# Optimization experiments

Hardware: AMD Instinct MI355X
Metric: run time of the kernel (lower is better)

Reference implementation:

```python
import jax, jax.numpy as jnp
import numpy as np

T, H, I, E, K = 4096, 1024, 768, 8, 2

def setup_inputs() -> dict:
    key = jax.random.key(0)
    k1, k2, k3, k4 = jax.random.split(key, 4)
    s_h = 1.0 / np.sqrt(H)
    s_i = 1.0 / np.sqrt(I)
    return {
        "hidden_states": jax.random.normal(k1, (T, H), dtype=jnp.float32),
        "gate_w": jax.random.normal(k2, (E, H), dtype=jnp.float32) * s_h,   # router, fp32
        "w13": jax.random.normal(k3, (E, 2 * I, H), dtype=jnp.float32) * s_h,  # fused gate+up
        "w2": jax.random.normal(k4, (E, H, I), dtype=jnp.float32) * s_i,
        "num_global_tokens": T,
        "max_num_tokens_per_gpu": T,
    }

def reference(hidden_states, gate_w, w13, w2, num_global_tokens, max_num_tokens_per_gpu):
    x = hidden_states  # [T, H]
    orig_dtype = x.dtype
    # router runs in fp32 (router_dtype == 'float32')
    router_logits = jnp.einsum('th,eh->te', x.astype(jnp.float32), gate_w)
    router_logits = router_logits.astype(orig_dtype)
    # FusedMoE top-k: softmax in fp32 over all experts, then top-k; renormalize=False
    probs = jax.nn.softmax(router_logits.astype(jnp.float32), axis=-1)  # [T, E]
    topk_w, topk_ids = jax.lax.top_k(probs, K)  # [T, K]
    # dense combine weights [T, E] (scatter of top-k weights)
    combine = jnp.sum(jax.nn.one_hot(topk_ids, E, dtype=topk_w.dtype) * topk_w[..., None], axis=1)
    combine = combine.astype(orig_dtype)
    # dense per-expert SwiGLU MLP, masked-combined (grouped GEMM reference)
    h = jnp.einsum('th,ejh->tej', x, w13)  # [T, E, 2I]
    g, u = h[..., :I], h[..., I:]
    a = jax.nn.silu(g) * u                 # [T, E, I]
    o = jnp.einsum('tei,ehi->teh', a, w2)  # [T, E, H]
    out = jnp.einsum('teh,te->th', o, combine)  # routed_scaling_factor = 1.0
    return out.reshape(x.shape)
```

## Files before the change

### kernel.cpp

```cpp
#include <hip/hip_runtime.h>
#include <hip/hip_bf16.h>

#define TT 4096
#define HH 1024
#define II 768
#define EE 8
#define TWOI 1536

typedef __attribute__((ext_vector_type(8))) short bf16x8;
typedef __attribute__((ext_vector_type(8))) unsigned short u16x8;
typedef __attribute__((ext_vector_type(4))) float f32x4;

__device__ unsigned short g_x_bf[TT * HH];
__device__ unsigned short g_w13_bf[EE * TWOI * HH];
__device__ unsigned short g_w2_bf[EE * HH * II];
__device__ unsigned short g_a[EE * TT * II];
__device__ unsigned short g_opart[2 * TT * HH];
__device__ int g_perm_tok[EE * TT];
__device__ float g_perm_w[EE * TT];
__device__ int g_perm_slot[EE * TT];
__device__ int g_cnt[EE];
__device__ int g_e1[TT];
__device__ int g_e2[TT];
__device__ float g_w1f[TT];
__device__ float g_w2f[TT];

__device__ __forceinline__ unsigned short f2bf(float f) {
  union { float f; unsigned u; } v; v.f = f;
  unsigned r = v.u + 0x7fff + ((v.u >> 16) & 1);
  return (unsigned short)(r >> 16);
}

__device__ __forceinline__ float bf2f(unsigned short u) {
  union { unsigned v; float f; } c; c.v = (unsigned)u << 16; return c.f;
}

__device__ __forceinline__ void gload16(const void* g, void* l) {
  __builtin_amdgcn_global_load_lds(
      (const __attribute__((address_space(1))) void*)g,
      (__attribute__((address_space(3))) void*)l, 16, 0, 0);
}

__device__ __forceinline__ void cvt_sub(const float* __restrict__ inb,
                                        unsigned short* __restrict__ dstb,
                                        long rowbase, int nrowf,
                                        long chunkbase, char* lds) {
  const int tid = threadIdx.x;
  const int wv = tid >> 6;
  const int lane = tid & 63;
#pragma unroll
  for (int i = 0; i < 4; ++i) {
    int r = i * 4 + wv;
    const float* src = inb + (rowbase + r) * (size_t)nrowf + lane * 4;
    gload16(src, lds + r * 1040);
  }
  asm volatile("s_waitcnt vmcnt(0)" ::: "memory");
  __syncthreads();
#pragma unroll
  for (int it = 0; it < 2; ++it) {
    int kb = it * 4 + wv;
    int g = lane;
    int r = g & 15, c8 = g >> 4;
    const float* lf = (const float*)(lds + r * 1040) + kb * 32 + c8 * 8;
    float4 a = ((const float4*)lf)[0];
    float4 c = ((const float4*)lf)[1];
    u16x8 o;
    o[0] = f2bf(a.x); o[1] = f2bf(a.y); o[2] = f2bf(a.z); o[3] = f2bf(a.w);
    o[4] = f2bf(c.x); o[5] = f2bf(c.y); o[6] = f2bf(c.z); o[7] = f2bf(c.w);
    *(u16x8*)(dstb + (chunkbase + kb) * 512 + (size_t)g * 8) = o;
  }
}

__global__ __launch_bounds__(256) void k_prep(const float* __restrict__ x,
                                              const float* __restrict__ gw,
                                              const float* __restrict__ w13,
                                              const float* __restrict__ w2) {
  __shared__ char lds[16640];
  const int b = blockIdx.x;
  const int wv = threadIdx.x >> 6;
  const int lane = threadIdx.x & 63;
  if (b >= 1024) {
    if (b < 4096) {
      int s = b - 1024;
      int grp = s >> 2, sub = s & 3;
      cvt_sub(w13 + sub * 256, g_w13_bf, (long)grp * 16, HH,
              (long)grp * 32 + sub * 8, lds);
    } else {
      int s = b - 4096;
      int grp = s / 3, sub = s - grp * 3;
      cvt_sub(w2 + sub * 256, g_w2_bf, (long)grp * 16, II,
              (long)grp * 24 + sub * 8, lds);
    }
    return;
  }
  const int t = b * 4 + wv;

  const float* xr = x + (size_t)t * HH + lane * 16;
  float4 xv0 = *(const float4*)(xr + 0);
  float4 xv1 = *(const float4*)(xr + 4);
  float4 xv2 = *(const float4*)(xr + 8);
  float4 xv3 = *(const float4*)(xr + 12);

  unsigned short* xd = g_x_bf + (size_t)t * HH + lane * 16;
  ushort4 o0, o1, o2, o3;
  o0.x = f2bf(xv0.x); o0.y = f2bf(xv0.y); o0.z = f2bf(xv0.z); o0.w = f2bf(xv0.w);
  o1.x = f2bf(xv1.x); o1.y = f2bf(xv1.y); o1.z = f2bf(xv1.z); o1.w = f2bf(xv1.w);
  o2.x = f2bf(xv2.x); o2.y = f2bf(xv2.y); o2.z = f2bf(xv2.z); o2.w = f2bf(xv2.w);
  o3.x = f2bf(xv3.x); o3.y = f2bf(xv3.y); o3.z = f2bf(xv3.z); o3.w = f2bf(xv3.w);
  *(ushort4*)(xd + 0) = o0;
  *(ushort4*)(xd + 4) = o1;
  *(ushort4*)(xd + 8) = o2;
  *(ushort4*)(xd + 12) = o3;

  float lg[EE];
#pragma unroll
  for (int ei = 0; ei < EE; ++ei) {
    const float* gr = gw + ei * HH + lane * 16;
    float4 g0 = *(const float4*)(gr + 0);
    float4 g1 = *(const float4*)(gr + 4);
    float4 g2 = *(const float4*)(gr + 8);
    float4 g3 = *(const float4*)(gr + 12);
    float a = xv0.x * g0.x + xv0.y * g0.y + xv0.z * g0.z + xv0.w * g0.w
            + xv1.x * g1.x + xv1.y * g1.y + xv1.z * g1.z + xv1.w * g1.w
            + xv2.x * g2.x + xv2.y * g2.y + xv2.z * g2.z + xv2.w * g2.w
            + xv3.x * g3.x + xv3.y * g3.y + xv3.z * g3.z + xv3.w * g3.w;
#pragma unroll
    for (int s = 32; s > 0; s >>= 1) a += __shfl_xor(a, s);
    lg[ei] = a;
  }

  if (lane == 0) {
    float mx = lg[0];
#pragma unroll
    for (int ei = 1; ei < EE; ++ei) mx = fmaxf(mx, lg[ei]);
    float p[EE]; float s = 0.f;
#pragma unroll
    for (int ei = 0; ei < EE; ++ei) { p[ei] = expf(lg[ei] - mx); s += p[ei]; }
    float inv = 1.f / s;
    int e1 = 0; float b1 = lg[0];
#pragma unroll
    for (int ei = 1; ei < EE; ++ei) if (lg[ei] > b1) { b1 = lg[ei]; e1 = ei; }
    int e2 = -1; float b2 = -3.0e38f;
#pragma unroll
    for (int ei = 0; ei < EE; ++ei)
      if (ei != e1 && lg[ei] > b2) { b2 = lg[ei]; e2 = ei; }

    g_e1[t] = e1;
    g_e2[t] = e2;
    g_w1f[t] = p[e1] * inv;
    g_w2f[t] = p[e2] * inv;
  }
}

__global__ __launch_bounds__(256) void k_compact() {
  const int e = blockIdx.x;
  const int tid = threadIdx.x;
  __shared__ int pre[256];

  const int t0 = tid * (TT / 256);
  int c = 0;
#pragma unroll
  for (int j = 0; j < TT / 256; ++j) {
    int t = t0 + j;
    if (g_e1[t] == e) ++c;
    if (g_e2[t] == e) ++c;
  }
  pre[tid] = c;
  __syncthreads();
  for (int off = 1; off < 256; off <<= 1) {
    int v = (tid >= off) ? pre[tid - off] : 0;
    __syncthreads();
    pre[tid] += v;
    __syncthreads();
  }
  int pos = pre[tid] - c;
#pragma unroll
  for (int j = 0; j < TT / 256; ++j) {
    int t = t0 + j;
    if (g_e1[t] == e) {
      g_perm_tok[e * TT + pos] = t;
      g_perm_w[e * TT + pos] = g_w1f[t];
      g_perm_slot[e * TT + pos] = 0;
      ++pos;
    }
    if (g_e2[t] == e) {
      g_perm_tok[e * TT + pos] = t;
      g_perm_w[e * TT + pos] = g_w2f[t];
      g_perm_slot[e * TT + pos] = 1;
      ++pos;
    }
  }
  if (tid == 255) g_cnt[e] = pre[255];
}

__global__ __launch_bounds__(512) void k_gemm1() {
  const int bid = blockIdx.x;
  const int e = bid & 7;
  const int k = bid >> 3;
  const int cb = k % 6;
  const int rowbase = (k / 6) * 128;
  const int cnt = g_cnt[e];
  if (rowbase >= cnt) return;
  const int tid = threadIdx.x;
  const int lane = tid & 63;
  const int wid = tid >> 6;
  const int wm = wid >> 1;
  const int wc = wid & 1;

  __shared__ uint4 sA[3][512];
  __shared__ uint4 sBg[3][512];
  __shared__ uint4 sBu[3][512];

  const int r16 = lane & 15;
  const int c8 = lane >> 4;
  const int arow = rowbase + wid * 16 + r16;
  const int tok = (arow < cnt) ? g_perm_tok[e * TT + arow] : 0;
  const unsigned short* aptr = g_x_bf + (size_t)tok * HH + c8 * 8;
  const unsigned short* bgp =
      g_w13_bf + ((size_t)(e * 96 + cb * 8 + wid) * 32) * 512 + lane * 8;
  const unsigned short* bup = bgp + (size_t)48 * 32 * 512;

  const int soff = __builtin_amdgcn_readfirstlane(wid * 1024);

#define STG1(buf, kk) do { \
    gload16(aptr + (kk) * 32, (char*)sA + (buf) * 8192 + soff); \
    gload16(bgp + (size_t)(kk) * 512, (char*)sBg + (buf) * 8192 + soff); \
    gload16(bup + (size_t)(kk) * 512, (char*)sBu + (buf) * 8192 + soff); \
  } while (0)

  f32x4 accg[2][4], accu[2][4];
#pragma unroll
  for (int m = 0; m < 2; ++m)
#pragma unroll
    for (int n = 0; n < 4; ++n) {
      accg[m][n] = (f32x4){0.f, 0.f, 0.f, 0.f};
      accu[m][n] = (f32x4){0.f, 0.f, 0.f, 0.f};
    }

  STG1(0, 0);
  STG1(1, 1);
  for (int ks = 0; ks < 32; ++ks) {
    const int cur = ks % 3;
    if (ks < 30) {
      const int stg = (ks + 2) % 3;
      STG1(stg, ks + 2);
      asm volatile("s_waitcnt vmcnt(6)" ::: "memory");
    } else if (ks == 30) {
      asm volatile("s_waitcnt vmcnt(3)" ::: "memory");
    } else {
      asm volatile("s_waitcnt vmcnt(0)" ::: "memory");
    }
    __builtin_amdgcn_s_barrier();
    __builtin_amdgcn_sched_barrier(0);
    bf16x8 af[2], bgf[4], buf_[4];
#pragma unroll
    for (int m = 0; m < 2; ++m)
      af[m] = *(const bf16x8*)((const char*)sA + cur * 8192 + (wm * 2 + m) * 1024 + lane * 16);
#pragma unroll
    for (int n = 0; n < 4; ++n) {
      int jb = wc * 4 + n;
      bgf[n] = *(const bf16x8*)((const char*)sBg + cur * 8192 + jb * 1024 + lane * 16);
      buf_[n] = *(const bf16x8*)((const char*)sBu + cur * 8192 + jb * 1024 + lane * 16);
    }
#pragma unroll
    for (int m = 0; m < 2; ++m)
#pragma unroll
      for (int n = 0; n < 4; ++n) {
        accg[m][n] = __builtin_amdgcn_mfma_f32_16x16x32_bf16(af[m], bgf[n], accg[m][n], 0, 0, 0);
        accu[m][n] = __builtin_amdgcn_mfma_f32_16x16x32_bf16(af[m], buf_[n], accu[m][n], 0, 0, 0);
      }
    __builtin_amdgcn_sched_barrier(0);
    __builtin_amdgcn_s_barrier();
  }
#undef STG1

  const int rhi = lane >> 4, clo = lane & 15;
  unsigned short* abase = g_a + ((size_t)(e * 256 + (rowbase >> 4)) * 24) * 512;
#pragma unroll
  for (int m = 0; m < 2; ++m) {
#pragma unroll
    for (int jj = 0; jj < 4; ++jj) {
      int rbl = wm * 2 + m;
      int rr = rhi * 4 + jj;
      int row = rowbase + rbl * 16 + rr;
      if (row < cnt) {
#pragma unroll
        for (int n = 0; n < 4; ++n) {
          int kb = cb * 4 + wc * 2 + (n >> 1);
          int sub = (2 * n + (clo >> 3)) & 3;
          float gv = accg[m][n][jj];
          float uv = accu[m][n][jj];
          float av = gv / (1.f + __expf(-gv)) * uv;
          abase[((size_t)rbl * 24 + kb) * 512 + sub * 128 + rr * 8 + (clo & 7)] = f2bf(av);
        }
      }
    }
  }
}

__global__ __launch_bounds__(512) void k_gemm2() {
  const int bid = blockIdx.x;
  const int e = bid & 7;
  const int k = bid >> 3;
  const int cb = k % 8;
  const int rowbase = (k / 8) * 128;
  const int cnt = g_cnt[e];
  if (rowbase >= cnt) return;
  const int tid = threadIdx.x;
  const int lane = tid & 63;
  const int wid = tid >> 6;
  const int wm = wid >> 1;
  const int wc = wid & 1;

  __shared__ uint4 sA[3][512];
  __shared__ uint4 sB[3][512];
  __shared__ int s_tok[128];
  __shared__ float s_w[128];
  __shared__ int s_slot[128];

  if (tid < 128) {
    int row = rowbase + tid;
    bool v = row < cnt;
    s_tok[tid] = v ? g_perm_tok[e * TT + row] : 0;
    s_w[tid] = v ? g_perm_w[e * TT + row] : 0.f;
    s_slot[tid] = v ? g_perm_slot[e * TT + row] : 0;
  }

  const unsigned short* aptr =
      g_a + ((size_t)(e * 256 + (rowbase >> 4) + wid) * 24) * 512 + lane * 8;
  const unsigned short* bp =
      g_w2_bf + ((size_t)(e * 64 + cb * 8 + wid) * 24) * 512 + lane * 8;

  const int soff = __builtin_amdgcn_readfirstlane(wid * 1024);

#define STG2(buf, kk) do { \
    gload16(aptr + (size_t)(kk) * 512, (char*)sA + (buf) * 8192 + soff); \
    gload16(bp + (size_t)(kk) * 512, (char*)sB + (buf) * 8192 + soff); \
  } while (0)

  f32x4 acc[2][4];
#pragma unroll
  for (int m = 0; m < 2; ++m)
#pragma unroll
    for (int n = 0; n < 4; ++n) acc[m][n] = (f32x4){0.f, 0.f, 0.f, 0.f};

  STG2(0, 0);
  STG2(1, 1);
  for (int ks = 0; ks < 24; ++ks) {
    const int cur = ks % 3;
    if (ks < 22) {
      const int stg = (ks + 2) % 3;
      STG2(stg, ks + 2);
      asm volatile("s_waitcnt vmcnt(4)" ::: "memory");
    } else if (ks == 22) {
      asm volatile("s_waitcnt vmcnt(2)" ::: "memory");
    } else {
      asm volatile("s_waitcnt vmcnt(0)" ::: "memory");
    }
    __builtin_amdgcn_s_barrier();
    __builtin_amdgcn_sched_barrier(0);
    bf16x8 af[2], bfr[4];
#pragma unroll
    for (int m = 0; m < 2; ++m)
      af[m] = *(const bf16x8*)((const char*)sA + cur * 8192 + (wm * 2 + m) * 1024 + lane * 16);
#pragma unroll
    for (int n = 0; n < 4; ++n)
      bfr[n] = *(const bf16x8*)((const char*)sB + cur * 8192 + (wc * 4 + n) * 1024 + lane * 16);
#pragma unroll
    for (int m = 0; m < 2; ++m)
#pragma unroll
      for (int n = 0; n < 4; ++n)
        acc[m][n] = __builtin_amdgcn_mfma_f32_16x16x32_bf16(af[m], bfr[n], acc[m][n], 0, 0, 0);
    __builtin_amdgcn_sched_barrier(0);
    __builtin_amdgcn_s_barrier();
  }
#undef STG2

  const int rhi = lane >> 4, clo = lane & 15;
#pragma unroll
  for (int m = 0; m < 2; ++m) {
#pragma unroll
    for (int jj = 0; jj < 4; ++jj) {
      int rloc = wm * 32 + m * 16 + rhi * 4 + jj;
      if (rowbase + rloc < cnt) {
        int tok = s_tok[rloc];
        float w = s_w[rloc];
        unsigned short* orow =
            g_opart + (size_t)s_slot[rloc] * TT * HH + (size_t)tok * HH;
#pragma unroll
        for (int n = 0; n < 4; ++n) {
          int h2 = cb * 128 + wc * 64 + n * 16 + clo;
          orow[h2] = f2bf(w * acc[m][n][jj]);
        }
      }
    }
  }
}

__global__ __launch_bounds__(256) void k_combine(float* __restrict__ out) {
  int idx = (blockIdx.x * 256 + threadIdx.x) * 8;
  u16x8 p0 = *(const u16x8*)(g_opart + idx);
  u16x8 p1 = *(const u16x8*)(g_opart + TT * HH + idx);
  float4 o0, o1;
  o0.x = bf2f(p0[0]) + bf2f(p1[0]);
  o0.y = bf2f(p0[1]) + bf2f(p1[1]);
  o0.z = bf2f(p0[2]) + bf2f(p1[2]);
  o0.w = bf2f(p0[3]) + bf2f(p1[3]);
  o1.x = bf2f(p0[4]) + bf2f(p1[4]);
  o1.y = bf2f(p0[5]) + bf2f(p1[5]);
  o1.z = bf2f(p0[6]) + bf2f(p1[6]);
  o1.w = bf2f(p0[7]) + bf2f(p1[7]);
  *(float4*)(out + idx) = o0;
  *(float4*)(out + idx + 4) = o1;
}

extern "C" void kernel_launch(void* const* d_in, const int* in_sizes, int n_in,
                              void* d_out, int out_size, void* d_ws, size_t ws_size,
                              hipStream_t stream) {
  (void)in_sizes; (void)n_in; (void)d_ws; (void)ws_size; (void)out_size;
  const float* x   = (const float*)d_in[0];
  const float* gw  = (const float*)d_in[1];
  const float* w13 = (const float*)d_in[2];
  const float* w2  = (const float*)d_in[3];
  float* out = (float*)d_out;

  k_prep<<<dim3(5632), dim3(256), 0, stream>>>(x, gw, w13, w2);
  k_compact<<<dim3(EE), dim3(256), 0, stream>>>();
  k_gemm1<<<dim3(480), dim3(512), 0, stream>>>();
  k_gemm2<<<dim3(640), dim3(512), 0, stream>>>();
  k_combine<<<dim3(TT * HH / 2048), dim3(256), 0, stream>>>(out);
}
```

Before: 113.0 us.

## Persist weight-conversion blocks over nine chunks with double-buffered LDS DMA

New measurement: 113.5 us. Within noise of the previous version (+0.4%).

```diff
diff --git a/kernel.cpp b/kernel.cpp
--- a/kernel.cpp
+++ b/kernel.cpp
@@ -41,33 +41,58 @@
       (__attribute__((address_space(3))) void*)l, 16, 0, 0);
 }
 
-__device__ __forceinline__ void cvt_sub(const float* __restrict__ inb,
-                                        unsigned short* __restrict__ dstb,
-                                        long rowbase, int nrowf,
-                                        long chunkbase, char* lds) {
-  const int tid = threadIdx.x;
-  const int wv = tid >> 6;
-  const int lane = tid & 63;
-#pragma unroll
-  for (int i = 0; i < 4; ++i) {
-    int r = i * 4 + wv;
-    const float* src = inb + (rowbase + r) * (size_t)nrowf + lane * 4;
-    gload16(src, lds + r * 1040);
-  }
-  asm volatile("s_waitcnt vmcnt(0)" ::: "memory");
-  __syncthreads();
+struct SubDesc {
+  const float* src;
+  unsigned short* dst;
+  long cb;
+  int nrowf;
+};
+
+__device__ __forceinline__ SubDesc sub_desc(int s, const float* w13,
+                                            const float* w2) {
+  SubDesc d;
+  if (s < 3072) {
+    int grp = s >> 2, sb = s & 3;
+    d.src = w13 + (size_t)grp * 16 * HH + sb * 256;
+    d.dst = g_w13_bf;
+    d.cb = (long)grp * 32 + sb * 8;
+    d.nrowf = HH;
+  } else {
+    int s2 = s - 3072;
+    int grp = s2 / 3, sb = s2 - grp * 3;
+    d.src = w2 + (size_t)grp * 16 * II + sb * 256;
+    d.dst = g_w2_bf;
+    d.cb = (long)grp * 24 + sb * 8;
+    d.nrowf = II;
+  }
+  return d;
+}
+
+__device__ __forceinline__ void cvt_dma(const float* src, int nrowf, char* lds) {
+  const int wv = threadIdx.x >> 6;
+  const int lane = threadIdx.x & 63;
+#pragma unroll
+  for (int j = 0; j < 4; ++j) {
+    int r = j * 4 + wv;
+    gload16(src + (size_t)r * nrowf + lane * 4, lds + r * 1040);
+  }
+}
+
+__device__ __forceinline__ void cvt_emit(unsigned short* dstb, long chunkbase,
+                                         const char* lds) {
+  const int wv = threadIdx.x >> 6;
+  const int lane = threadIdx.x & 63;
 #pragma unroll
   for (int it = 0; it < 2; ++it) {
     int kb = it * 4 + wv;
-    int g = lane;
-    int r = g & 15, c8 = g >> 4;
+    int r = lane & 15, c8 = lane >> 4;
     const float* lf = (const float*)(lds + r * 1040) + kb * 32 + c8 * 8;
     float4 a = ((const float4*)lf)[0];
     float4 c = ((const float4*)lf)[1];
     u16x8 o;
     o[0] = f2bf(a.x); o[1] = f2bf(a.y); o[2] = f2bf(a.z); o[3] = f2bf(a.w);
     o[4] = f2bf(c.x); o[5] = f2bf(c.y); o[6] = f2bf(c.z); o[7] = f2bf(c.w);
-    *(u16x8*)(dstb + (chunkbase + kb) * 512 + (size_t)g * 8) = o;
+    *(u16x8*)(dstb + (chunkbase + kb) * 512 + (size_t)lane * 8) = o;
   }
 }
 
@@ -75,21 +100,30 @@
                                               const float* __restrict__ gw,
                                               const float* __restrict__ w13,
                                               const float* __restrict__ w2) {
-  __shared__ char lds[16640];
+  __shared__ char lds[2][16640];
   const int b = blockIdx.x;
   const int wv = threadIdx.x >> 6;
   const int lane = threadIdx.x & 63;
   if (b >= 1024) {
-    if (b < 4096) {
-      int s = b - 1024;
-      int grp = s >> 2, sub = s & 3;
-      cvt_sub(w13 + sub * 256, g_w13_bf, (long)grp * 16, HH,
-              (long)grp * 32 + sub * 8, lds);
-    } else {
-      int s = b - 4096;
-      int grp = s / 3, sub = s - grp * 3;
-      cvt_sub(w2 + sub * 256, g_w2_bf, (long)grp * 16, II,
-              (long)grp * 24 + sub * 8, lds);
+    const int base = (b - 1024) * 9;
+    SubDesc d0 = sub_desc(base, w13, w2);
+    cvt_dma(d0.src, d0.nrowf, lds[0]);
+#pragma unroll 1
+    for (int i = 0; i < 9; ++i) {
+      SubDesc dc = sub_desc(base + i, w13, w2);
+      if (i < 8) {
+        SubDesc dn = sub_desc(base + i + 1, w13, w2);
+        cvt_dma(dn.src, dn.nrowf, lds[(i + 1) & 1]);
+        if (i == 0) asm volatile("s_waitcnt vmcnt(4)" ::: "memory");
+        else        asm volatile("s_waitcnt vmcnt(6)" ::: "memory");
+      } else {
+        asm volatile("s_waitcnt vmcnt(2)" ::: "memory");
+      }
+      __builtin_amdgcn_s_barrier();
+      __builtin_amdgcn_sched_barrier(0);
+      cvt_emit(dc.dst, dc.cb, lds[i & 1]);
+      __builtin_amdgcn_sched_barrier(0);
+      __builtin_amdgcn_s_barrier();
     }
     return;
   }
@@ -424,7 +458,7 @@
   const float* w2  = (const float*)d_in[3];
   float* out = (float*)d_out;
 
-  k_prep<<<dim3(5632), dim3(256), 0, stream>>>(x, gw, w13, w2);
+  k_prep<<<dim3(1536), dim3(256), 0, stream>>>(x, gw, w13, w2);
   k_compact<<<dim3(EE), dim3(256), 0, stream>>>();
   k_gemm1<<<dim3(480), dim3(512), 0, stream>>>();
   k_gemm2<<<dim3(640), dim3(512), 0, stream>>>();
```
